# Optimization experiments

Hardware: AMD Instinct MI355X
Metric: run time of the kernel (lower is better)

The kernel has to match this reference:

```python
import jax, jax.numpy as jnp
import numpy as np

SIGMA_P = 1.0
SIGMA_I = 9.0


def setup_inputs() -> dict:
    key = jax.random.key(0)
    k1, k2, k3, k4 = jax.random.split(key, 4)
    batch, n_samples = 4096, 8192
    # per-batch public signal scalar, std = sigma_P (broadcast over n_samples in reference)
    pub_sign = jax.random.normal(k1, (batch,), dtype=jnp.float32) * SIGMA_P
    # per-(batch, sample) private signal, std = sigma_I
    priv_sign = jax.random.normal(k2, (batch, n_samples, 1), dtype=jnp.float32) * SIGMA_I
    param_b = jax.random.normal(k3, (1, 1), dtype=jnp.float32)
    param_c = jax.random.normal(k4, (1, 1), dtype=jnp.float32)
    return {"pub_sign": pub_sign, "priv_sign": priv_sign, "param_b": param_b, "param_c": param_c}


def reference(pub_sign, priv_sign, param_b, param_c):
    # signal: (batch, n_samples, 1); pub_sign scalar broadcast over samples
    signal = pub_sign[:, None, None] * param_b + priv_sign * param_c
    signal = jnp.clip(signal, -20.0, 20.0)
    # 2*exp(s)/(1+exp(s)) - 1 == 2*sigmoid(s) - 1 (stable form)
    signal = 2.0 * jax.nn.sigmoid(signal) - 1.0
    return jnp.mean(signal, axis=1, keepdims=True)  # (batch, 1, 1)
```

## Files before the change

kernel.cpp:

```cpp
#include <hip/hip_runtime.h>

#define N_SAMPLES 8192
#define BLOCK 256
#define VEC 4
#define ITERS (N_SAMPLES / (BLOCK * VEC))

typedef float f32x4 __attribute__((ext_vector_type(4)));

__global__ __launch_bounds__(BLOCK) void noise_layer_kernel(
    const float* __restrict__ pub_sign,
    const float* __restrict__ priv_sign,
    const float* __restrict__ param_b,
    const float* __restrict__ param_c,
    float* __restrict__ out)
{
    const int b = blockIdx.x;
    const float B = param_b[0];
    const float C = param_c[0];

    const float L2E   = 1.44269504088896340736f;
    const float CL    = C * L2E;
    const float baseL = pub_sign[b] * B * L2E;
    const float LIM   = 20.0f * L2E;

    const f32x4* row = reinterpret_cast<const f32x4*>(
        priv_sign + (size_t)b * N_SAMPLES);

    f32x4 v[ITERS];
#pragma unroll
    for (int i = 0; i < ITERS; ++i)
        v[i] = row[threadIdx.x + i * BLOCK];

    float r_sum = 0.0f;
#pragma unroll
    for (int i = 0; i < ITERS; ++i) {
#pragma unroll
        for (int j = 0; j < 4; ++j) {
            float s2 = fmaf(v[i][j], CL, baseL);
            s2 = fminf(LIM, fmaxf(-LIM, s2));
            float e = exp2f(s2);
            r_sum += __builtin_amdgcn_rcpf(1.0f + e);
        }
    }

#pragma unroll
    for (int off = 32; off > 0; off >>= 1)
        r_sum += __shfl_down(r_sum, off, 64);

    __shared__ float part[BLOCK / 64];
    const int wave = threadIdx.x >> 6;
    const int lane = threadIdx.x & 63;
    if (lane == 0) part[wave] = r_sum;
    __syncthreads();

    if (threadIdx.x == 0) {
        float t = 0.0f;
#pragma unroll
        for (int w = 0; w < BLOCK / 64; ++w) t += part[w];
        out[b] = 1.0f - t * (1.0f / (float)(N_SAMPLES / 2));
    }
}

extern "C" void kernel_launch(void* const* d_in, const int* in_sizes, int n_in,
                              void* d_out, int out_size, void* d_ws, size_t ws_size,
                              hipStream_t stream) {
    const float* pub_sign  = (const float*)d_in[0];
    const float* priv_sign = (const float*)d_in[1];
    const float* param_b   = (const float*)d_in[2];
    const float* param_c   = (const float*)d_in[3];
    float* out = (float*)d_out;

    const int batch = in_sizes[0];
    noise_layer_kernel<<<batch, BLOCK, 0, stream>>>(
        pub_sign, priv_sign, param_b, param_c, out);
}
```

Measured before the change: 192.4 us.

## Pair sigmoid reciprocals algebraically and stream nontemporal vector loads per iteration

Combines pairs of 1/(1+e) terms into a single (2+e0+e1)/((1+e0)(1+e1)) so that one reciprocal serves two samples, halving rcp instructions. The loads switch to nontemporal per-iteration loads instead of preloading all vectors into registers, and the affine transform and clamp are vectorized. With the clamp at 20, the product of exponentials stays within float range, though rounding differs slightly. Dropping the preload may reduce memory-level parallelism unless the compiler hoists the loads.

```diff
diff --git a/kernel.cpp b/kernel.cpp
--- a/kernel.cpp
+++ b/kernel.cpp
@@ -15,32 +15,38 @@
     float* __restrict__ out)
 {
     const int b = blockIdx.x;
-    const float B = param_b[0];
-    const float C = param_c[0];
 
     const float L2E   = 1.44269504088896340736f;
-    const float CL    = C * L2E;
-    const float baseL = pub_sign[b] * B * L2E;
+    const float CL    = param_c[0] * L2E;
+    const float baseL = pub_sign[b] * param_b[0] * L2E;
     const float LIM   = 20.0f * L2E;
 
     const f32x4* row = reinterpret_cast<const f32x4*>(
         priv_sign + (size_t)b * N_SAMPLES);
 
-    f32x4 v[ITERS];
-#pragma unroll
-    for (int i = 0; i < ITERS; ++i)
-        v[i] = row[threadIdx.x + i * BLOCK];
+    const f32x4 CL4   = {CL, CL, CL, CL};
+    const f32x4 base4 = {baseL, baseL, baseL, baseL};
+    const f32x4 lim4  = {LIM, LIM, LIM, LIM};
+    const f32x4 nlim4 = {-LIM, -LIM, -LIM, -LIM};
 
     float r_sum = 0.0f;
 #pragma unroll
     for (int i = 0; i < ITERS; ++i) {
-#pragma unroll
-        for (int j = 0; j < 4; ++j) {
-            float s2 = fmaf(v[i][j], CL, baseL);
-            s2 = fminf(LIM, fmaxf(-LIM, s2));
-            float e = exp2f(s2);
-            r_sum += __builtin_amdgcn_rcpf(1.0f + e);
-        }
+        f32x4 v = __builtin_nontemporal_load(&row[threadIdx.x + i * BLOCK]);
+        f32x4 s = v * CL4 + base4;
+        s = __builtin_elementwise_min(lim4, __builtin_elementwise_max(nlim4, s));
+
+        float e0 = exp2f(s[0]);
+        float e1 = exp2f(s[1]);
+        float e2 = exp2f(s[2]);
+        float e3 = exp2f(s[3]);
+
+        float t01 = e0 + e1;
+        float t23 = e2 + e3;
+        float d01 = fmaf(e0, e1, 1.0f + t01);
+        float d23 = fmaf(e2, e3, 1.0f + t23);
+        r_sum += (2.0f + t01) * __builtin_amdgcn_rcpf(d01);
+        r_sum += (2.0f + t23) * __builtin_amdgcn_rcpf(d23);
     }
 
 #pragma unroll
```

Measured after the change: 183.9 us. 4.4% less time.
